# Kernel tuning notes

Measured on AMD Instinct MI355X. Metric: run time of the kernel, lower is better.

Reference implementation:

```python
import jax, jax.numpy as jnp
import numpy as np

B, C, H, W = 256, 512, 14, 14  # C = rnn_size
S = 7                          # spp_size

def setup_inputs() -> dict:
    key = jax.random.key(0)
    ks = jax.random.split(key, 8)
    sd = 1.0 / np.sqrt(C)
    return {
        "att_v": jax.random.normal(ks[0], (B, C, H, W), dtype=jnp.float32),
        "h": jax.random.normal(ks[1], (B, C), dtype=jnp.float32),
        # a2a: Linear(rnn_size, rnn_size)
        "Wa": jax.random.uniform(ks[2], (C, C), jnp.float32, -sd, sd),
        "ba": jax.random.uniform(ks[3], (C,), jnp.float32, -sd, sd),
        # h2a: Linear(rnn_size, rnn_size)
        "Wh": jax.random.uniform(ks[4], (C, C), jnp.float32, -sd, sd),
        "bh": jax.random.uniform(ks[5], (C,), jnp.float32, -sd, sd),
        # d2d: Linear(rnn_size, 1)
        "Wd": jax.random.uniform(ks[6], (C,), jnp.float32, -sd, sd),
        "bd": jax.random.uniform(ks[7], (1,), jnp.float32, -sd, sd),
    }

def reference(att_v, h, Wa, ba, Wh, bh, Wd, bd):
    b, c, hh, ww = att_v.shape
    # AdaptiveAvgPool2d(S) with H,W divisible by S -> block mean
    pooled = att_v.reshape(b, c, S, hh // S, S, ww // S).mean(axis=(3, 5))  # [B,C,S,S]
    a = pooled.reshape(b, c, S * S).transpose(0, 2, 1)  # [B, N=49, C]
    av = jnp.einsum('bnc,dc->bnd', a, Wa) + ba          # a2a, torch Linear: x @ W.T + b
    ah = h @ Wh.T + bh                                  # h2a, [B,C]
    dot = jnp.tanh(av + ah[:, None, :])                 # broadcast add + tanh
    scores = jnp.einsum('bnd,d->bn', dot, Wd) + bd[0]   # d2d -> [B, N]
    weight = jax.nn.softmax(scores, axis=-1)            # over attention positions
    att_res = jnp.einsum('bnc,bn->bc', a, weight)       # bmm(att^T, weight)
    return att_res
```

## Files before the change

kernel.cpp:

```cpp
#include <hip/hip_runtime.h>
#include <hip/hip_bf16.h>

#define BATCH 256
#define CDIM  512
#define NPOS  49
#define NPAD  64
#define ASTRIDE 520

typedef __attribute__((ext_vector_type(8))) short bf16x8_t;
typedef __attribute__((ext_vector_type(4))) float f32x4_t;

#define WS_NEED 18153472u

__global__ __launch_bounds__(256) void prep(
    const float* __restrict__ Wa, const float* __restrict__ Wh,
    const float* __restrict__ h,
    __hip_bfloat16* __restrict__ Wab, __hip_bfloat16* __restrict__ Whb,
    __hip_bfloat16* __restrict__ hb, float* __restrict__ scores) {
    int gid = blockIdx.x * 256 + threadIdx.x;
    if (gid < 163840) {
        const float* src; __hip_bfloat16* dst; int idx;
        if (gid < 65536)       { src = Wa; dst = Wab; idx = gid; }
        else if (gid < 131072) { src = Wh; dst = Whb; idx = gid - 65536; }
        else                   { src = h;  dst = hb;  idx = gid - 131072; }
        float4 v = ((const float4*)src)[idx];
        dst[idx * 4 + 0] = __float2bfloat16(v.x);
        dst[idx * 4 + 1] = __float2bfloat16(v.y);
        dst[idx * 4 + 2] = __float2bfloat16(v.z);
        dst[idx * 4 + 3] = __float2bfloat16(v.w);
    } else {
        int idx = gid - 163840;
        ((float4*)scores)[idx] = (float4){0.f, 0.f, 0.f, 0.f};
    }
}

__global__ __launch_bounds__(256, 6) void pool_kernel(
    const float* __restrict__ att_v, __hip_bfloat16* __restrict__ pooled) {
    __shared__ float4 lds[32 * 49];
    const int b  = blockIdx.x >> 4;
    const int cg = blockIdx.x & 15;
    const int t  = threadIdx.x;

    const float4* src = (const float4*)(att_v + ((size_t)b * CDIM + cg * 32) * 196);
    #pragma unroll
    for (int k = 0; k < 7; ++k) {
        int idx = t + k * 256;
        if (idx < 1568) lds[idx] = src[idx];
    }
    __syncthreads();

    const int i = t >> 5;
    const int c = t & 31;
    if (i < 7) {
        const float4* fp = &lds[c * 49 + 7 * i];
        float4 f0 = fp[0], f1 = fp[1], f2 = fp[2], f3 = fp[3];
        float4 f4 = fp[4], f5 = fp[5], f6 = fp[6];
        float p[7];
        p[0] = f0.x + f0.y + f3.z + f3.w;
        p[1] = f0.z + f0.w + f4.x + f4.y;
        p[2] = f1.x + f1.y + f4.z + f4.w;
        p[3] = f1.z + f1.w + f5.x + f5.y;
        p[4] = f2.x + f2.y + f5.z + f5.w;
        p[5] = f2.z + f2.w + f6.x + f6.y;
        p[6] = f3.x + f3.y + f6.z + f6.w;
        __hip_bfloat16* outp = pooled + (size_t)b * NPAD * CDIM + cg * 32 + c;
        #pragma unroll
        for (int j = 0; j < 7; ++j)
            outp[(size_t)(i * 7 + j) * CDIM] = __float2bfloat16(p[j] * 0.25f);
    }
}

__global__ __launch_bounds__(256, 4) void gemm_score(
    const __hip_bfloat16* __restrict__ pooled,
    const __hip_bfloat16* __restrict__ Wab,
    const __hip_bfloat16* __restrict__ Whb,
    const __hip_bfloat16* __restrict__ hb,
    const float* __restrict__ ba, const float* __restrict__ bh,
    const float* __restrict__ Wd, float* __restrict__ scores) {
    __shared__ float s_lds[NPAD];
    const int b    = blockIdx.x >> 2;
    const int jt   = blockIdx.x & 3;
    const int wave = threadIdx.x >> 6;
    const int lane = threadIdx.x & 63;
    const int q = lane >> 4;
    const int r = lane & 15;

    if (threadIdx.x < NPAD) s_lds[threadIdx.x] = 0.f;

    const int d0 = jt * 128 + wave * 32 + r;
    const __hip_bfloat16* Ap = pooled + (size_t)b * NPAD * CDIM;
    const __hip_bfloat16* hp = hb + (size_t)b * CDIM;

    f32x4_t acc[4][2];
    #pragma unroll
    for (int rt = 0; rt < 4; ++rt)
        #pragma unroll
        for (int ct = 0; ct < 2; ++ct)
            acc[rt][ct] = (f32x4_t){0.f, 0.f, 0.f, 0.f};

    #pragma unroll 4
    for (int ks = 0; ks < 16; ++ks) {
        const int k0 = ks * 32 + q * 8;
        bf16x8_t af[4], bf[2];
        #pragma unroll
        for (int rt = 0; rt < 4; ++rt)
            af[rt] = *(const bf16x8_t*)&Ap[(size_t)(rt * 16 + r) * CDIM + k0];
        #pragma unroll
        for (int ct = 0; ct < 2; ++ct)
            bf[ct] = *(const bf16x8_t*)&Wab[(size_t)(d0 + 16 * ct) * CDIM + k0];
        #pragma unroll
        for (int rt = 0; rt < 4; ++rt)
            #pragma unroll
            for (int ct = 0; ct < 2; ++ct)
                acc[rt][ct] = __builtin_amdgcn_mfma_f32_16x16x32_bf16(
                    af[rt], bf[ct], acc[rt][ct], 0, 0, 0);
    }
    #pragma unroll 4
    for (int ks = 0; ks < 16; ++ks) {
        const int k0 = ks * 32 + q * 8;
        bf16x8_t ah = *(const bf16x8_t*)&hp[k0];
        bf16x8_t bf[2];
        #pragma unroll
        for (int ct = 0; ct < 2; ++ct)
            bf[ct] = *(const bf16x8_t*)&Whb[(size_t)(d0 + 16 * ct) * CDIM + k0];
        #pragma unroll
        for (int rt = 0; rt < 4; ++rt)
            #pragma unroll
            for (int ct = 0; ct < 2; ++ct)
                acc[rt][ct] = __builtin_amdgcn_mfma_f32_16x16x32_bf16(
                    ah, bf[ct], acc[rt][ct], 0, 0, 0);
    }

    float part[4][4];
    #pragma unroll
    for (int rt = 0; rt < 4; ++rt)
        #pragma unroll
        for (int rg = 0; rg < 4; ++rg) part[rt][rg] = 0.f;
    #pragma unroll
    for (int ct = 0; ct < 2; ++ct) {
        const int d = d0 + 16 * ct;
        const float bias = ba[d] + bh[d];
        const float wd = Wd[d];
        #pragma unroll
        for (int rt = 0; rt < 4; ++rt)
            #pragma unroll
            for (int rg = 0; rg < 4; ++rg) {
                float x = acc[rt][ct][rg] + bias;
                float e = __expf(2.f * x);
                part[rt][rg] += (1.f - 2.f / (e + 1.f)) * wd;
            }
    }
    #pragma unroll
    for (int m = 1; m < 16; m <<= 1)
        #pragma unroll
        for (int rt = 0; rt < 4; ++rt)
            #pragma unroll
            for (int rg = 0; rg < 4; ++rg)
                part[rt][rg] += __shfl_xor(part[rt][rg], m, 64);
    __syncthreads();
    if (r == 0) {
        #pragma unroll
        for (int rt = 0; rt < 4; ++rt)
            #pragma unroll
            for (int rg = 0; rg < 4; ++rg)
                atomicAdd(&s_lds[rt * 16 + q * 4 + rg], part[rt][rg]);
    }
    __syncthreads();
    if (threadIdx.x < NPAD)
        atomicAdd(&scores[b * NPAD + threadIdx.x], s_lds[threadIdx.x]);
}

__global__ __launch_bounds__(256) void softmax_wsum(
    const float* __restrict__ scores, const __hip_bfloat16* __restrict__ pooled,
    float* __restrict__ out) {
    const int b  = blockIdx.x >> 1;
    const int ch = (blockIdx.x & 1) * 256 + threadIdx.x;
    const float* sp = scores + b * NPAD;
    float vmax = -3.0e38f;
    #pragma unroll
    for (int n = 0; n < NPOS; ++n) vmax = fmaxf(vmax, sp[n]);
    const __hip_bfloat16* Ap = pooled + (size_t)b * NPAD * CDIM + ch;
    float sum = 0.f, accv = 0.f;
    #pragma unroll
    for (int n = 0; n < NPOS; ++n) {
        float e = __expf(sp[n] - vmax);
        sum += e;
        accv += e * __bfloat162float(Ap[(size_t)n * CDIM]);
    }
    out[b * CDIM + ch] = accv / sum;
}

__global__ void prep_convert(const float* __restrict__ Wa,
                             const float* __restrict__ Wh,
                             __hip_bfloat16* __restrict__ Wab,
                             __hip_bfloat16* __restrict__ Whb) {
    int gid = blockIdx.x * blockDim.x + threadIdx.x;
    const int quarter = (CDIM * CDIM) / 4;
    const float4* src; __hip_bfloat16* dst; int idx;
    if (gid < quarter) { src = (const float4*)Wa; dst = Wab; idx = gid; }
    else               { src = (const float4*)Wh; dst = Whb; idx = gid - quarter; }
    float4 v = src[idx];
    dst[idx * 4 + 0] = __float2bfloat16(v.x);
    dst[idx * 4 + 1] = __float2bfloat16(v.y);
    dst[idx * 4 + 2] = __float2bfloat16(v.z);
    dst[idx * 4 + 3] = __float2bfloat16(v.w);
}

__global__ __launch_bounds__(512, 2) void att_spp_main(
    const float* __restrict__ att_v, const float* __restrict__ h,
    const float* __restrict__ ba, const float* __restrict__ bh,
    const float* __restrict__ Wd,
    const __hip_bfloat16* __restrict__ Wab, const __hip_bfloat16* __restrict__ Whb,
    float* __restrict__ out) {
    __shared__ __hip_bfloat16 a_lds[NPAD * ASTRIDE];
    __shared__ __hip_bfloat16 h_lds[CDIM];
    __shared__ float babh_lds[CDIM];
    __shared__ float wd_lds[CDIM];
    __shared__ float scores_lds[NPAD];
    __shared__ float weights_lds[NPOS];
    const int b = blockIdx.x, t = threadIdx.x;
    h_lds[t]    = __float2bfloat16(h[b * CDIM + t]);
    babh_lds[t] = ba[t] + bh[t];
    wd_lds[t]   = Wd[t];
    if (t < NPAD) scores_lds[t] = 0.f;
    for (int idx = t; idx < (NPAD - NPOS) * ASTRIDE; idx += 512)
        a_lds[NPOS * ASTRIDE + idx] = __float2bfloat16(0.f);
    {
        const int jj = t & 7, g = t >> 3;
        const float2* att2 = (const float2*)(att_v + (size_t)b * CDIM * 196);
        if (jj < 7) {
            for (int ci = 0; ci < 8; ++ci) {
                const int c = g + (ci << 6), cbase = c * 98;
                #pragma unroll
                for (int i = 0; i < 7; ++i) {
                    float2 v0 = att2[cbase + i * 14 + jj];
                    float2 v1 = att2[cbase + i * 14 + 7 + jj];
                    a_lds[(i * 7 + jj) * ASTRIDE + c] =
                        __float2bfloat16((v0.x + v0.y + v1.x + v1.y) * 0.25f);
                }
            }
        }
    }
    __syncthreads();
    const int wave = t >> 6, lane = t & 63, q = lane >> 4, r = lane & 15;
    f32x4_t acc[4][4];
    #pragma unroll
    for (int rt = 0; rt < 4; ++rt)
        #pragma unroll
        for (int ct = 0; ct < 4; ++ct) acc[rt][ct] = (f32x4_t){0.f,0.f,0.f,0.f};
    const int dBase = wave * 64 + r;
    for (int ks = 0; ks < 16; ++ks) {
        const int k0 = ks * 32 + q * 8;
        bf16x8_t af[4], bf[4];
        #pragma unroll
        for (int rt = 0; rt < 4; ++rt)
            af[rt] = *(const bf16x8_t*)&a_lds[(rt * 16 + r) * ASTRIDE + k0];
        #pragma unroll
        for (int ct = 0; ct < 4; ++ct)
            bf[ct] = *(const bf16x8_t*)&Wab[(size_t)(dBase + ct * 16) * CDIM + k0];
        #pragma unroll
        for (int rt = 0; rt < 4; ++rt)
            #pragma unroll
            for (int ct = 0; ct < 4; ++ct)
                acc[rt][ct] = __builtin_amdgcn_mfma_f32_16x16x32_bf16(
                    af[rt], bf[ct], acc[rt][ct], 0, 0, 0);
    }
    for (int ks = 0; ks < 16; ++ks) {
        const int k0 = ks * 32 + q * 8;
        bf16x8_t af = *(const bf16x8_t*)&h_lds[k0];
        bf16x8_t bf[4];
        #pragma unroll
        for (int ct = 0; ct < 4; ++ct)
            bf[ct] = *(const bf16x8_t*)&Whb[(size_t)(dBase + ct * 16) * CDIM + k0];
        #pragma unroll
        for (int rt = 0; rt < 4; ++rt)
            #pragma unroll
            for (int ct = 0; ct < 4; ++ct)
                acc[rt][ct] = __builtin_amdgcn_mfma_f32_16x16x32_bf16(
                    af, bf[ct], acc[rt][ct], 0, 0, 0);
    }
    float part[4][4];
    #pragma unroll
    for (int rt = 0; rt < 4; ++rt)
        #pragma unroll
        for (int rg = 0; rg < 4; ++rg) part[rt][rg] = 0.f;
    #pragma unroll
    for (int ct = 0; ct < 4; ++ct) {
        const int d = dBase + ct * 16;
        const float bias = babh_lds[d], wd = wd_lds[d];
        #pragma unroll
        for (int rt = 0; rt < 4; ++rt)
            #pragma unroll
            for (int rg = 0; rg < 4; ++rg) {
                float x = acc[rt][ct][rg] + bias;
                float e = __expf(2.f * x);
                part[rt][rg] += (1.f - 2.f / (e + 1.f)) * wd;
            }
    }
    #pragma unroll
    for (int m = 1; m < 16; m <<= 1)
        #pragma unroll
        for (int rt = 0; rt < 4; ++rt)
            #pragma unroll
            for (int rg = 0; rg < 4; ++rg)
                part[rt][rg] += __shfl_xor(part[rt][rg], m, 64);
    if (r == 0) {
        #pragma unroll
        for (int rt = 0; rt < 4; ++rt)
            #pragma unroll
            for (int rg = 0; rg < 4; ++rg)
                atomicAdd(&scores_lds[rt * 16 + q * 4 + rg], part[rt][rg]);
    }
    __syncthreads();
    if (wave == 0) {
        float v = (lane < NPOS) ? scores_lds[lane] : -3.0e38f;
        float vmax = v;
        #pragma unroll
        for (int m = 1; m < 64; m <<= 1) vmax = fmaxf(vmax, __shfl_xor(vmax, m, 64));
        float e = (lane < NPOS) ? __expf(v - vmax) : 0.f;
        float s = e;
        #pragma unroll
        for (int m = 1; m < 64; m <<= 1) s += __shfl_xor(s, m, 64);
        if (lane < NPOS) weights_lds[lane] = e / s;
    }
    __syncthreads();
    float sum = 0.f;
    #pragma unroll
    for (int n = 0; n < NPOS; ++n)
        sum += __bfloat162float(a_lds[n * ASTRIDE + t]) * weights_lds[n];
    out[b * CDIM + t] = sum;
}

extern "C" void kernel_launch(void* const* d_in, const int* in_sizes, int n_in,
                              void* d_out, int out_size, void* d_ws, size_t ws_size,
                              hipStream_t stream) {
    const float* att_v = (const float*)d_in[0];
    const float* h     = (const float*)d_in[1];
    const float* Wa    = (const float*)d_in[2];
    const float* ba    = (const float*)d_in[3];
    const float* Wh    = (const float*)d_in[4];
    const float* bh    = (const float*)d_in[5];
    const float* Wd    = (const float*)d_in[6];

    if (ws_size >= WS_NEED) {
        char* ws = (char*)d_ws;
        __hip_bfloat16* Wab    = (__hip_bfloat16*)(ws);
        __hip_bfloat16* Whb    = (__hip_bfloat16*)(ws + 524288);
        __hip_bfloat16* hb     = (__hip_bfloat16*)(ws + 1048576);
        __hip_bfloat16* pooled = (__hip_bfloat16*)(ws + 1310720);
        float*          scores = (float*)(ws + 18087936);

        prep<<<656, 256, 0, stream>>>(Wa, Wh, h, Wab, Whb, hb, scores);
        pool_kernel<<<4096, 256, 0, stream>>>(att_v, pooled);
        gemm_score<<<1024, 256, 0, stream>>>(pooled, Wab, Whb, hb, ba, bh, Wd, scores);
        softmax_wsum<<<512, 256, 0, stream>>>(scores, pooled, (float*)d_out);
    } else {
        __hip_bfloat16* Wab = (__hip_bfloat16*)d_ws;
        __hip_bfloat16* Whb = Wab + (size_t)CDIM * CDIM;
        prep_convert<<<512, 256, 0, stream>>>(Wa, Wh, Wab, Whb);
        att_spp_main<<<BATCH, 512, 0, stream>>>(att_v, h, ba, bh, Wd, Wab, Whb,
                                                (float*)d_out);
    }
}
```

Before: 233.7 us.

## Restructure attention scoring into a flattened LDS-tiled GEMM with separate h2a GEMM

Drops the 64-row padding of pooled features and treats all batch positions as one 12544x512 matrix, tiled 128x128 through LDS using global_load_lds, so Wa tiles are reused across many batch rows instead of being re-read per batch. The h2a projection moves into its own small tiled GEMM that writes fp32 results plus bias, and the score kernel then adds that per batch row. The cost of padded rows and the redundant per-block h MFMA loop is removed, in exchange for an extra launch, an extra intermediate buffer, and per-row global atomics on scores.

```diff
diff --git a/kernel.cpp b/kernel.cpp
--- a/kernel.cpp
+++ b/kernel.cpp
@@ -4,13 +4,19 @@
 #define BATCH 256
 #define CDIM  512
 #define NPOS  49
-#define NPAD  64
+#define MROWS 12544
 #define ASTRIDE 520
 
 typedef __attribute__((ext_vector_type(8))) short bf16x8_t;
 typedef __attribute__((ext_vector_type(4))) float f32x4_t;
 
-#define WS_NEED 18153472u
+#define WS_NEED 14730240u
+
+__device__ __forceinline__ void load_lds16(const void* g, void* l) {
+    __builtin_amdgcn_global_load_lds(
+        (const __attribute__((address_space(1))) void*)g,
+        (__attribute__((address_space(3))) void*)l, 16, 0, 0);
+}
 
 __global__ __launch_bounds__(256) void prep(
     const float* __restrict__ Wa, const float* __restrict__ Wh,
@@ -18,6 +24,7 @@
     __hip_bfloat16* __restrict__ Wab, __hip_bfloat16* __restrict__ Whb,
     __hip_bfloat16* __restrict__ hb, float* __restrict__ scores) {
     int gid = blockIdx.x * 256 + threadIdx.x;
+    if (gid >= 166976) return;
     if (gid < 163840) {
         const float* src; __hip_bfloat16* dst; int idx;
         if (gid < 65536)       { src = Wa; dst = Wab; idx = gid; }
@@ -63,111 +70,164 @@
         p[4] = f2.x + f2.y + f5.z + f5.w;
         p[5] = f2.z + f2.w + f6.x + f6.y;
         p[6] = f3.x + f3.y + f6.z + f6.w;
-        __hip_bfloat16* outp = pooled + (size_t)b * NPAD * CDIM + cg * 32 + c;
+        __hip_bfloat16* outp = pooled + ((size_t)b * NPOS + i * 7) * CDIM + cg * 32 + c;
         #pragma unroll
         for (int j = 0; j < 7; ++j)
-            outp[(size_t)(i * 7 + j) * CDIM] = __float2bfloat16(p[j] * 0.25f);
-    }
-}
-
-__global__ __launch_bounds__(256, 4) void gemm_score(
-    const __hip_bfloat16* __restrict__ pooled,
-    const __hip_bfloat16* __restrict__ Wab,
-    const __hip_bfloat16* __restrict__ Whb,
-    const __hip_bfloat16* __restrict__ hb,
+            outp[(size_t)j * CDIM] = __float2bfloat16(p[j] * 0.25f);
+    }
+}
+
+__global__ __launch_bounds__(256, 2) void ah_gemm(
+    const __hip_bfloat16* __restrict__ A,
+    const __hip_bfloat16* __restrict__ Bw,
     const float* __restrict__ ba, const float* __restrict__ bh,
-    const float* __restrict__ Wd, float* __restrict__ scores) {
-    __shared__ float s_lds[NPAD];
-    const int b    = blockIdx.x >> 2;
-    const int jt   = blockIdx.x & 3;
-    const int wave = threadIdx.x >> 6;
-    const int lane = threadIdx.x & 63;
-    const int q = lane >> 4;
-    const int r = lane & 15;
-
-    if (threadIdx.x < NPAD) s_lds[threadIdx.x] = 0.f;
-
-    const int d0 = jt * 128 + wave * 32 + r;
-    const __hip_bfloat16* Ap = pooled + (size_t)b * NPAD * CDIM;
-    const __hip_bfloat16* hp = hb + (size_t)b * CDIM;
-
-    f32x4_t acc[4][2];
+    float* __restrict__ ahb) {
+    __shared__ __hip_bfloat16 aT[128 * 32];
+    __shared__ __hip_bfloat16 bT[128 * 32];
+    const int mt = blockIdx.x & 1;
+    const int nt = blockIdx.x >> 1;
+    const int t = threadIdx.x;
+    const int wave = t >> 6, lane = t & 63;
+    const int wm = wave & 1, wn = wave >> 1;
+    const int q = lane >> 4, r = lane & 15;
+    const int m0 = mt * 128, n0 = nt * 128;
+
+    const __hip_bfloat16* Ag = A + (size_t)(m0 + wave * 16 + (lane >> 2)) * CDIM + (lane & 3) * 8;
+    const __hip_bfloat16* Bg = Bw + (size_t)(n0 + wave * 16 + (lane >> 2)) * CDIM + (lane & 3) * 8;
+    char* aD = (char*)aT + wave * 1024 + lane * 16;
+    char* bD = (char*)bT + wave * 1024 + lane * 16;
+
+    f32x4_t acc[4][4];
     #pragma unroll
     for (int rt = 0; rt < 4; ++rt)
         #pragma unroll
-        for (int ct = 0; ct < 2; ++ct)
-            acc[rt][ct] = (f32x4_t){0.f, 0.f, 0.f, 0.f};
-
-    #pragma unroll 4
+        for (int ct = 0; ct < 4; ++ct) acc[rt][ct] = (f32x4_t){0.f, 0.f, 0.f, 0.f};
+
     for (int ks = 0; ks < 16; ++ks) {
-        const int k0 = ks * 32 + q * 8;
-        bf16x8_t af[4], bf[2];
-        #pragma unroll
-        for (int rt = 0; rt < 4; ++rt)
-            af[rt] = *(const bf16x8_t*)&Ap[(size_t)(rt * 16 + r) * CDIM + k0];
-        #pragma unroll
-        for (int ct = 0; ct < 2; ++ct)
-            bf[ct] = *(const bf16x8_t*)&Wab[(size_t)(d0 + 16 * ct) * CDIM + k0];
-        #pragma unroll
-        for (int rt = 0; rt < 4; ++rt)
-            #pragma unroll
-            for (int ct = 0; ct < 2; ++ct)
+        const __hip_bfloat16* ag = Ag + ks * 32;
+        const __hip_bfloat16* bg = Bg + ks * 32;
+        load_lds16(ag, aD);
+        load_lds16(ag + 64 * CDIM, aD + 4096);
+        load_lds16(bg, bD);
+        load_lds16(bg + 64 * CDIM, bD + 4096);
+        __syncthreads();
+        bf16x8_t af[4], bf[4];
+        #pragma unroll
+        for (int rt = 0; rt < 4; ++rt)
+            af[rt] = *(const bf16x8_t*)&aT[(wm * 64 + rt * 16 + r) * 32 + q * 8];
+        #pragma unroll
+        for (int ct = 0; ct < 4; ++ct)
+            bf[ct] = *(const bf16x8_t*)&bT[(wn * 64 + ct * 16 + r) * 32 + q * 8];
+        #pragma unroll
+        for (int rt = 0; rt < 4; ++rt)
+            #pragma unroll
+            for (int ct = 0; ct < 4; ++ct)
                 acc[rt][ct] = __builtin_amdgcn_mfma_f32_16x16x32_bf16(
                     af[rt], bf[ct], acc[rt][ct], 0, 0, 0);
-    }
-    #pragma unroll 4
+        __syncthreads();
+    }
+    #pragma unroll
+    for (int ct = 0; ct < 4; ++ct) {
+        const int col = n0 + wn * 64 + ct * 16 + r;
+        const float bias = ba[col] + bh[col];
+        #pragma unroll
+        for (int rt = 0; rt < 4; ++rt)
+            #pragma unroll
+            for (int rg = 0; rg < 4; ++rg) {
+                const int row = m0 + wm * 64 + rt * 16 + q * 4 + rg;
+                ahb[(size_t)row * CDIM + col] = acc[rt][ct][rg] + bias;
+            }
+    }
+}
+
+__global__ __launch_bounds__(256, 2) void gemm_score2(
+    const __hip_bfloat16* __restrict__ A,
+    const __hip_bfloat16* __restrict__ Bw,
+    const float* __restrict__ ahb,
+    const float* __restrict__ Wd,
+    float* __restrict__ scores) {
+    __shared__ __hip_bfloat16 aT[128 * 32];
+    __shared__ __hip_bfloat16 bT[128 * 32];
+    const int mt = blockIdx.x % 98;
+    const int nt = blockIdx.x / 98;
+    const int t = threadIdx.x;
+    const int wave = t >> 6, lane = t & 63;
+    const int wm = wave & 1, wn = wave >> 1;
+    const int q = lane >> 4, r = lane & 15;
+    const int m0 = mt * 128, n0 = nt * 128;
+
+    const __hip_bfloat16* Ag = A + (size_t)(m0 + wave * 16 + (lane >> 2)) * CDIM + (lane & 3) * 8;
+    const __hip_bfloat16* Bg = Bw + (size_t)(n0 + wave * 16 + (lane >> 2)) * CDIM + (lane & 3) * 8;
+    char* aD = (char*)aT + wave * 1024 + lane * 16;
+    char* bD = (char*)bT + wave * 1024 + lane * 16;
+
+    f32x4_t acc[4][4];
+    #pragma unroll
+    for (int rt = 0; rt < 4; ++rt)
+        #pragma unroll
+        for (int ct = 0; ct < 4; ++ct) acc[rt][ct] = (f32x4_t){0.f, 0.f, 0.f, 0.f};
+
     for (int ks = 0; ks < 16; ++ks) {
-        const int k0 = ks * 32 + q * 8;
-        bf16x8_t ah = *(const bf16x8_t*)&hp[k0];
-        bf16x8_t bf[2];
-        #pragma unroll
-        for (int ct = 0; ct < 2; ++ct)
-            bf[ct] = *(const bf16x8_t*)&Whb[(size_t)(d0 + 16 * ct) * CDIM + k0];
-        #pragma unroll
-        for (int rt = 0; rt < 4; ++rt)
-            #pragma unroll
-            for (int ct = 0; ct < 2; ++ct)
+        const __hip_bfloat16* ag = Ag + ks * 32;
+        const __hip_bfloat16* bg = Bg + ks * 32;
+        load_lds16(ag, aD);
+        load_lds16(ag + 64 * CDIM, aD + 4096);
+        load_lds16(bg, bD);
+        load_lds16(bg + 64 * CDIM, bD + 4096);
+        __syncthreads();
+        bf16x8_t af[4], bf[4];
+        #pragma unroll
+        for (int rt = 0; rt < 4; ++rt)
+            af[rt] = *(const bf16x8_t*)&aT[(wm * 64 + rt * 16 + r) * 32 + q * 8];
+        #pragma unroll
+        for (int ct = 0; ct < 4; ++ct)
+            bf[ct] = *(const bf16x8_t*)&bT[(wn * 64 + ct * 16 + r) * 32 + q * 8];
+        #pragma unroll
+        for (int rt = 0; rt < 4; ++rt)
+            #pragma unroll
+            for (int ct = 0; ct < 4; ++ct)
                 acc[rt][ct] = __builtin_amdgcn_mfma_f32_16x16x32_bf16(
-                    ah, bf[ct], acc[rt][ct], 0, 0, 0);
-    }
-
-    float part[4][4];
+                    af[rt], bf[ct], acc[rt][ct], 0, 0, 0);
+        __syncthreads();
+    }
+
+    int bb[16];
     #pragma unroll
     for (int rt = 0; rt < 4; ++rt)
         #pragma unroll
-        for (int rg = 0; rg < 4; ++rg) part[rt][rg] = 0.f;
-    #pragma unroll
-    for (int ct = 0; ct < 2; ++ct) {
-        const int d = d0 + 16 * ct;
-        const float bias = ba[d] + bh[d];
-        const float wd = Wd[d];
+        for (int rg = 0; rg < 4; ++rg)
+            bb[rt * 4 + rg] = (m0 + wm * 64 + rt * 16 + q * 4 + rg) / NPOS;
+
+    float rsum[16];
+    #pragma unroll
+    for (int i = 0; i < 16; ++i) rsum[i] = 0.f;
+
+    #pragma unroll
+    for (int ct = 0; ct < 4; ++ct) {
+        const int col = n0 + wn * 64 + ct * 16 + r;
+        const float wd = Wd[col];
         #pragma unroll
         for (int rt = 0; rt < 4; ++rt)
             #pragma unroll
             for (int rg = 0; rg < 4; ++rg) {
-                float x = acc[rt][ct][rg] + bias;
+                float x = acc[rt][ct][rg] + ahb[(size_t)bb[rt * 4 + rg] * CDIM + col];
                 float e = __expf(2.f * x);
-                part[rt][rg] += (1.f - 2.f / (e + 1.f)) * wd;
+                rsum[rt * 4 + rg] += (1.f - 2.f / (e + 1.f)) * wd;
             }
     }
     #pragma unroll
     for (int m = 1; m < 16; m <<= 1)
         #pragma unroll
+        for (int i = 0; i < 16; ++i)
+            rsum[i] += __shfl_xor(rsum[i], m, 64);
+    if (r == 0) {
+        #pragma unroll
         for (int rt = 0; rt < 4; ++rt)
             #pragma unroll
             for (int rg = 0; rg < 4; ++rg)
-                part[rt][rg] += __shfl_xor(part[rt][rg], m, 64);
-    __syncthreads();
-    if (r == 0) {
-        #pragma unroll
-        for (int rt = 0; rt < 4; ++rt)
-            #pragma unroll
-            for (int rg = 0; rg < 4; ++rg)
-                atomicAdd(&s_lds[rt * 16 + q * 4 + rg], part[rt][rg]);
-    }
-    __syncthreads();
-    if (threadIdx.x < NPAD)
-        atomicAdd(&scores[b * NPAD + threadIdx.x], s_lds[threadIdx.x]);
+                atomicAdd(&scores[m0 + wm * 64 + rt * 16 + q * 4 + rg],
+                          rsum[rt * 4 + rg]);
+    }
 }
 
 __global__ __launch_bounds__(256) void softmax_wsum(
@@ -175,11 +235,11 @@
     float* __restrict__ out) {
     const int b  = blockIdx.x >> 1;
     const int ch = (blockIdx.x & 1) * 256 + threadIdx.x;
-    const float* sp = scores + b * NPAD;
+    const float* sp = scores + b * NPOS;
     float vmax = -3.0e38f;
     #pragma unroll
     for (int n = 0; n < NPOS; ++n) vmax = fmaxf(vmax, sp[n]);
-    const __hip_bfloat16* Ap = pooled + (size_t)b * NPAD * CDIM + ch;
+    const __hip_bfloat16* Ap = pooled + (size_t)b * NPOS * CDIM + ch;
     float sum = 0.f, accv = 0.f;
     #pragma unroll
     for (int n = 0; n < NPOS; ++n) {
@@ -212,18 +272,18 @@
     const float* __restrict__ Wd,
     const __hip_bfloat16* __restrict__ Wab, const __hip_bfloat16* __restrict__ Whb,
     float* __restrict__ out) {
-    __shared__ __hip_bfloat16 a_lds[NPAD * ASTRIDE];
+    __shared__ __hip_bfloat16 a_lds[64 * ASTRIDE];
     __shared__ __hip_bfloat16 h_lds[CDIM];
     __shared__ float babh_lds[CDIM];
     __shared__ float wd_lds[CDIM];
-    __shared__ float scores_lds[NPAD];
+    __shared__ float scores_lds[64];
     __shared__ float weights_lds[NPOS];
     const int b = blockIdx.x, t = threadIdx.x;
     h_lds[t]    = __float2bfloat16(h[b * CDIM + t]);
     babh_lds[t] = ba[t] + bh[t];
     wd_lds[t]   = Wd[t];
-    if (t < NPAD) scores_lds[t] = 0.f;
-    for (int idx = t; idx < (NPAD - NPOS) * ASTRIDE; idx += 512)
+    if (t < 64) scores_lds[t] = 0.f;
+    for (int idx = t; idx < (64 - NPOS) * ASTRIDE; idx += 512)
         a_lds[NPOS * ASTRIDE + idx] = __float2bfloat16(0.f);
     {
         const int jj = t & 7, g = t >> 3;
@@ -348,11 +408,13 @@
         __hip_bfloat16* Whb    = (__hip_bfloat16*)(ws + 524288);
         __hip_bfloat16* hb     = (__hip_bfloat16*)(ws + 1048576);
         __hip_bfloat16* pooled = (__hip_bfloat16*)(ws + 1310720);
-        float*          scores = (float*)(ws + 18087936);
-
-        prep<<<656, 256, 0, stream>>>(Wa, Wh, h, Wab, Whb, hb, scores);
+        float*          ahb    = (float*)(ws + 14155776);
+        float*          scores = (float*)(ws + 14680064);
+
+        prep<<<653, 256, 0, stream>>>(Wa, Wh, h, Wab, Whb, hb, scores);
         pool_kernel<<<4096, 256, 0, stream>>>(att_v, pooled);
-        gemm_score<<<1024, 256, 0, stream>>>(pooled, Wab, Whb, hb, ba, bh, Wd, scores);
+        ah_gemm<<<8, 256, 0, stream>>>(hb, Whb, ba, bh, ahb);
+        gemm_score2<<<392, 256, 0, stream>>>(pooled, Wab, ahb, Wd, scores);
         softmax_wsum<<<512, 256, 0, stream>>>(scores, pooled, (float*)d_out);
     } else {
         __hip_bfloat16* Wab = (__hip_bfloat16*)d_ws;
```

Result: faster. 200.6 us (-14.2%).
